# Optimization experiments

Measured on AMD Instinct MI355X. Metric: run time of the kernel, lower is better.

The kernel has to match this reference:

```python
import jax, jax.numpy as jnp
import numpy as np

B, N, S, K, NDIM, HID = 2, 8192, 1024, 32, 3, 256


def _sincos_embed(pos, dim):
    # pos: (..., ndim) continuous coordinates -> (..., dim) sincos embedding
    ndim = pos.shape[-1]
    emb_dim_per_dim = dim // ndim
    half = emb_dim_per_dim // 2
    freq = jnp.exp(jnp.arange(half, dtype=pos.dtype) * (-np.log(10000.0) / (half - 1)))
    embs = []
    for i in range(ndim):
        e = pos[..., i:i + 1] * freq  # (..., half)
        embs.append(jnp.concatenate([jnp.sin(e), jnp.cos(e)], axis=-1))
    x = jnp.concatenate(embs, axis=-1)  # (..., ndim*2*half)
    pad = dim - x.shape[-1]
    if pad > 0:
        x = jnp.pad(x, [(0, 0)] * (x.ndim - 1) + [(0, pad)])
    return x


def setup_inputs() -> dict:
    key = jax.random.key(0)
    ks = jax.random.split(key, 8)
    input_pos = jax.random.normal(ks[0], (B, N, NDIM), dtype=jnp.float32)
    supernode_idxs = jax.random.randint(ks[1], (S,), 0, N)
    # lecun_normal-style init (stddev = 1/sqrt(fan_in)), zero bias (torch/flax Dense default bias=0)
    w_in = jax.random.normal(ks[2], (NDIM, HID), dtype=jnp.float32) / np.sqrt(NDIM)
    b_in = jnp.zeros((HID,), jnp.float32)
    w1 = jax.random.normal(ks[3], (HID, HID), dtype=jnp.float32) / np.sqrt(HID)
    b1 = jnp.zeros((HID,), jnp.float32)
    w2 = jax.random.normal(ks[4], (HID, HID), dtype=jnp.float32) / np.sqrt(HID)
    b2 = jnp.zeros((HID,), jnp.float32)
    return {"input_pos": input_pos, "supernode_idxs": supernode_idxs,
            "w_in": w_in, "b_in": b_in, "w1": w1, "b1": b1, "w2": w2, "b2": b2}


def reference(input_pos, supernode_idxs, w_in, b_in, w1, b1, w2, b2):
    def knn(x):  # x: (N, ndim)
        # Euclidean distance from each supernode to every point: (S, N).
        # Same values as rows of the full NxN cdist the original materializes.
        d = jnp.sqrt(jnp.sum((x[supernode_idxs][:, None, :] - x[None, :, :]) ** 2, axis=-1))
        nbr = jnp.argsort(d, axis=1)[:, :K]  # (S, K)
        return x[nbr]  # (S, K, ndim)

    coords = jax.vmap(knn)(input_pos)  # (B, S, K, ndim)
    proj = coords @ w_in + b_in                         # (B, S, K, HID)
    pe = _sincos_embed(coords, HID)                     # (B, S, K, HID)
    h = proj + pe
    h = jax.nn.gelu(h @ w1 + b1) @ w2 + b2              # message MLP
    return jnp.mean(h, axis=-2)                         # (B, S, HID)
```

## Files before the change

kernel.cpp:

```cpp
#include <hip/hip_runtime.h>
#include <hip/hip_bf16.h>
#include <math.h>

#define BB   2
#define NN   8192
#define SS   1024
#define KK   32
#define HID  256
#define NTH  256
#define PPT  32
#define SENT 0xFFFFFFFFFFFFFFFFULL
#define LDB  264
#define WFE  65536

typedef unsigned long long u64;
typedef unsigned int       u32;
typedef short bf16x8 __attribute__((ext_vector_type(8)));
typedef float f32x4  __attribute__((ext_vector_type(4)));

#define CSW(SI) { const u64 mn = x < (SI) ? x : (SI); const u64 mx = x < (SI) ? (SI) : x; (SI) = mn; x = mx; }
#define INS(KV) { u64 x = (KV); CSW(s0) CSW(s1) CSW(s2) CSW(s3) }

__device__ __forceinline__ float tanh_fast(float y) {
    const float e = __expf(2.0f * y);
    const float r = __builtin_amdgcn_rcpf(e + 1.0f);
    return fmaf(-2.0f, r, 1.0f);
}

__device__ __forceinline__ short bf_bits(float f) {
    const __hip_bfloat16 h = __float2bfloat16(f);
    short s;
    __builtin_memcpy(&s, &h, 2);
    return s;
}

__device__ __forceinline__ int mbcnt64(u64 m) {
    return (int)__builtin_amdgcn_mbcnt_hi((u32)(m >> 32),
           __builtin_amdgcn_mbcnt_lo((u32)m, 0u));
}

__global__ void prep_w(const float* __restrict__ w1, const float* __restrict__ w2,
                       __hip_bfloat16* __restrict__ wf) {
    const int idx = blockIdx.x * 256 + threadIdx.x;
    const int j   = idx & 7;
    const int l   = (idx >> 3) & 63;
    const int ntg = (idx >> 9) & 15;
    const int ks  = (idx >> 13) & 7;
    const int mat = idx >> 16;
    const int k = ks * 32 + (l >> 4) * 8 + j;
    const int n = ntg * 16 + (l & 15);
    const float v = (mat ? w2 : w1)[k * HID + n];
    const __hip_bfloat16 hi = __float2bfloat16(v);
    const float res = v - __bfloat162float(hi);
    const size_t s0 = (size_t)mat * 131072 + ((size_t)((ks*16 + ntg)*2) * 64 + l) * 8 + j;
    wf[s0]       = hi;
    wf[s0 + 512] = __float2bfloat16(res);
}

__global__ __launch_bounds__(NTH, 8)
void snp_kernel(const float* __restrict__ pos,
                const int*   __restrict__ snidx,
                const float* __restrict__ w_in,
                const float* __restrict__ b_in,
                const float* __restrict__ b1,
                const float* __restrict__ b2,
                const __hip_bfloat16* __restrict__ wf,
                float*       __restrict__ out)
{
    const int bs   = blockIdx.x;
    const int b    = bs / SS;
    const int s    = bs - b * SS;
    const int t    = threadIdx.x;
    const int lane = t & 63;
    const int wv   = t >> 6;

    __shared__ __align__(16) short h0b[KK][LDB];
    __shared__ u64   wl[4 * KK];
    __shared__ int   nbr[KK];
    __shared__ __align__(16) float nbc[4 * KK];

    const float* posb = pos + (size_t)b * (NN * 3);
    const int   sp = snidx[s];
    const float sx = posb[sp*3 + 0];
    const float sy = posb[sp*3 + 1];
    const float sz = posb[sp*3 + 2];

    u64 s0=SENT,s1=SENT,s2=SENT,s3=SENT;
#pragma unroll 4
    for (int c = 0; c < PPT; ++c) {
        const int i = c * NTH + t;
        const float dx = __fsub_rn(sx, posb[i*3 + 0]);
        const float dy = __fsub_rn(sy, posb[i*3 + 1]);
        const float dz = __fsub_rn(sz, posb[i*3 + 2]);
        const float sq = __fadd_rn(__fadd_rn(__fmul_rn(dx,dx), __fmul_rn(dy,dy)),
                                   __fmul_rn(dz,dz));
        const u64 kv = ((u64)__float_as_uint(__fsqrt_rn(sq)) << 13) | (u32)i;
        INS(kv);
    }

    {
        u64 L = 0;
        for (int bit = 43; bit >= 13; --bit) {
            const u64 cand = L | (1ull << bit);
            const int cnt = __popcll(__ballot(s0 < cand)) + __popcll(__ballot(s1 < cand))
                          + __popcll(__ballot(s2 < cand)) + __popcll(__ballot(s3 < cand));
            if (cnt < 32) L = cand;
        }
        u64 TH = L + (1ull << 13);
        {
            const int cnt = __popcll(__ballot(s0 < TH)) + __popcll(__ballot(s1 < TH))
                          + __popcll(__ballot(s2 < TH)) + __popcll(__ballot(s3 < TH));
            if (cnt != 32) {
                for (int bit = 12; bit >= 0; --bit) {
                    const u64 cand = L | (1ull << bit);
                    const int c2 = __popcll(__ballot(s0 < cand)) + __popcll(__ballot(s1 < cand))
                                 + __popcll(__ballot(s2 < cand)) + __popcll(__ballot(s3 < cand));
                    if (c2 < 32) L = cand;
                }
                TH = L + 1;
            }
        }
        const bool b0 = s0 < TH, b1 = s1 < TH, b2 = s2 < TH, b3 = s3 < TH;
        const int csel = (int)b0 + (int)b1 + (int)b2 + (int)b3;

        if (__ballot(csel == 4) != 0ull) {
            int nv = 4;
#pragma unroll 1
            for (int it = 0; it < KK; ++it) {
                u64 m = s0;
#pragma unroll
                for (int off = 32; off > 0; off >>= 1) {
                    const u64 o = __shfl_xor(m, off, 64);
                    m = o < m ? o : m;
                }
                if (lane == 0) wl[wv*KK + it] = m;
                if (s0 == m) {
                    s0=s1; s1=s2; s2=s3; s3=SENT;
                    if (--nv == 0) {
                        const u64 last = m;
                        s0=s1=s2=s3=SENT;
#pragma unroll 4
                        for (int c = 0; c < PPT; ++c) {
                            const int i = c * NTH + t;
                            const float dx = __fsub_rn(sx, posb[i*3 + 0]);
                            const float dy = __fsub_rn(sy, posb[i*3 + 1]);
                            const float dz = __fsub_rn(sz, posb[i*3 + 2]);
                            const float sq = __fadd_rn(__fadd_rn(__fmul_rn(dx,dx), __fmul_rn(dy,dy)),
                                                       __fmul_rn(dz,dz));
                            u64 kv = ((u64)__float_as_uint(__fsqrt_rn(sq)) << 13) | (u32)i;
                            kv = kv > last ? kv : SENT;
                            INS(kv);
                        }
                        nv = (int)(s0!=SENT)+(int)(s1!=SENT)+(int)(s2!=SENT)+(int)(s3!=SENT);
                    }
                }
            }
        } else {
            const u64 m0 = __ballot(b0), m1 = __ballot(b1),
                      m2 = __ballot(b2), m3 = __ballot(b3);
            const int pos2 = mbcnt64(m0) + mbcnt64(m1) + mbcnt64(m2) + mbcnt64(m3);
            u64* wwl = &wl[wv * KK];
            if (b0) wwl[pos2]     = s0;
            if (b1) wwl[pos2 + 1] = s1;
            if (b2) wwl[pos2 + 2] = s2;
            if (b3) wwl[pos2 + 3] = s3;
        }
    }
    __syncthreads();

    if (t < 64) {
        const u64 k0 = wl[lane], k1 = wl[64 + lane];
        u64 L = 0;
        for (int bit = 43; bit >= 13; --bit) {
            const u64 cand = L | (1ull << bit);
            const int cnt = __popcll(__ballot(k0 < cand)) + __popcll(__ballot(k1 < cand));
            if (cnt < 32) L = cand;
        }
        u64 TH = L + (1ull << 13);
        {
            const int cnt = __popcll(__ballot(k0 < TH)) + __popcll(__ballot(k1 < TH));
            if (cnt != 32) {
                for (int bit = 12; bit >= 0; --bit) {
                    const u64 cand = L | (1ull << bit);
                    const int c2 = __popcll(__ballot(k0 < cand)) + __popcll(__ballot(k1 < cand));
                    if (c2 < 32) L = cand;
                }
                TH = L + 1;
            }
        }
        const bool c0 = k0 < TH, c1 = k1 < TH;
        const int p = mbcnt64(__ballot(c0)) + mbcnt64(__ballot(c1));
        if (c0) nbr[p]            = (int)(k0 & 8191u);
        if (c1) nbr[p + (int)c0]  = (int)(k1 & 8191u);
    }
    __syncthreads();

    if (t < KK * 3) {
        const int k = t / 3, d = t - 3 * k;
        nbc[k * 4 + d] = posb[(size_t)nbr[k] * 3 + d];
    }
    __syncthreads();

    {
        const int  c     = t;
        const int  dimi  = c / 84;
        const int  cc    = c - dimi * 84;
        const bool hasPe = c < 252;
        const bool isCos = cc >= 42;
        const int  f     = isCos ? cc - 42 : cc;
        const float fcoef = (float)(-9.210340371976184 / 41.0);
        const float freqv = expf((float)f * fcoef);
        const int  di    = hasPe ? dimi : 0;

        const float wi0 = w_in[0*HID + c];
        const float wi1 = w_in[1*HID + c];
        const float wi2 = w_in[2*HID + c];
        const float bi  = b_in[c];

#pragma unroll 4
        for (int k = 0; k < KK; ++k) {
            const float4 xv4 = *(const float4*)&nbc[k * 4];
            const float x0 = xv4.x, x1 = xv4.y, x2 = xv4.z;
            float v = fmaf(x2, wi2, fmaf(x1, wi1, fmaf(x0, wi0, bi)));
            if (hasPe) {
                const float xv  = (di == 0) ? x0 : ((di == 1) ? x1 : x2);
                const float ang = xv * freqv;
                v += isCos ? __cosf(ang) : __sinf(ang);
            }
            h0b[k][c] = bf_bits(v);
        }
    }
    __syncthreads();

    const int lr = lane & 15;
    const int lg = lane >> 4;
    const int nbase = wv * 64;

    const short* arow0 = &h0b[lr][lg * 8];
    const short* arow1 = &h0b[16 + lr][lg * 8];
    const __hip_bfloat16* wb1 = wf + (size_t)wv * 4096 + lane * 8;
    const __hip_bfloat16* wb2 = wb1 + 2 * WFE;

    f32x4 acc[2][4];

    {
#pragma unroll
        for (int nt = 0; nt < 4; ++nt) {
            const float bias = b1[nbase + nt*16 + lr];
            const f32x4 bv = {bias, bias, bias, bias};
            acc[0][nt] = bv; acc[1][nt] = bv;
        }
#pragma unroll 1
        for (int ks = 0; ks < 8; ++ks) {
            const bf16x8 af0 = *(const bf16x8*)(arow0 + ks * 32);
            const bf16x8 af1 = *(const bf16x8*)(arow1 + ks * 32);
            const __hip_bfloat16* p = wb1 + ks * 16384;
#pragma unroll
            for (int nt = 0; nt < 4; ++nt) {
                const bf16x8 bh = *(const bf16x8*)(p + nt * 1024);
                acc[0][nt] = __builtin_amdgcn_mfma_f32_16x16x32_bf16(af0, bh, acc[0][nt], 0,0,0);
                acc[1][nt] = __builtin_amdgcn_mfma_f32_16x16x32_bf16(af1, bh, acc[1][nt], 0,0,0);
                const bf16x8 bl = *(const bf16x8*)(p + nt * 1024 + 512);
                acc[0][nt] = __builtin_amdgcn_mfma_f32_16x16x32_bf16(af0, bl, acc[0][nt], 0,0,0);
                acc[1][nt] = __builtin_amdgcn_mfma_f32_16x16x32_bf16(af1, bl, acc[1][nt], 0,0,0);
            }
        }
    }
    __syncthreads();

    {
        const float kA = 0.7978845608028654f;
#pragma unroll
        for (int mt = 0; mt < 2; ++mt)
#pragma unroll
        for (int nt = 0; nt < 4; ++nt)
#pragma unroll
        for (int r = 0; r < 4; ++r) {
            const float x  = acc[mt][nt][r];
            const float x3 = x * x * x;
            const float tv = tanh_fast(kA * fmaf(0.044715f, x3, x));
            h0b[mt*16 + lg*4 + r][nbase + nt*16 + lr] = bf_bits(0.5f * x * (1.0f + tv));
        }
    }
    __syncthreads();

    {
        const f32x4 z = {0.f, 0.f, 0.f, 0.f};
#pragma unroll
        for (int nt = 0; nt < 4; ++nt) { acc[0][nt] = z; acc[1][nt] = z; }
#pragma unroll 1
        for (int ks = 0; ks < 8; ++ks) {
            const bf16x8 af0 = *(const bf16x8*)(arow0 + ks * 32);
            const bf16x8 af1 = *(const bf16x8*)(arow1 + ks * 32);
            const __hip_bfloat16* p = wb2 + ks * 16384;
#pragma unroll
            for (int nt = 0; nt < 4; ++nt) {
                const bf16x8 bh = *(const bf16x8*)(p + nt * 1024);
                acc[0][nt] = __builtin_amdgcn_mfma_f32_16x16x32_bf16(af0, bh, acc[0][nt], 0,0,0);
                acc[1][nt] = __builtin_amdgcn_mfma_f32_16x16x32_bf16(af1, bh, acc[1][nt], 0,0,0);
                const bf16x8 bl = *(const bf16x8*)(p + nt * 1024 + 512);
                acc[0][nt] = __builtin_amdgcn_mfma_f32_16x16x32_bf16(af0, bl, acc[0][nt], 0,0,0);
                acc[1][nt] = __builtin_amdgcn_mfma_f32_16x16x32_bf16(af1, bl, acc[1][nt], 0,0,0);
            }
        }
    }

#pragma unroll
    for (int nt = 0; nt < 4; ++nt) {
        float ssum = 0.0f;
#pragma unroll
        for (int mt = 0; mt < 2; ++mt)
#pragma unroll
            for (int r = 0; r < 4; ++r) ssum += acc[mt][nt][r];
        ssum += __shfl_xor(ssum, 16, 64);
        ssum += __shfl_xor(ssum, 32, 64);
        if (lane < 16) {
            const int ch = nbase + nt*16 + lane;
            out[(size_t)bs * HID + ch] = fmaf(ssum, 1.0f / KK, b2[ch]);
        }
    }
}

extern "C" void kernel_launch(void* const* d_in, const int* in_sizes, int n_in,
                              void* d_out, int out_size, void* d_ws, size_t ws_size,
                              hipStream_t stream) {
    const float* pos  = (const float*)d_in[0];
    const int*   sni  = (const int*)  d_in[1];
    const float* w_in = (const float*)d_in[2];
    const float* b_in = (const float*)d_in[3];
    const float* w1   = (const float*)d_in[4];
    const float* b1   = (const float*)d_in[5];
    const float* w2   = (const float*)d_in[6];
    const float* b2   = (const float*)d_in[7];
    float* out = (float*)d_out;
    __hip_bfloat16* wf = (__hip_bfloat16*)d_ws;
    (void)ws_size; (void)in_sizes; (void)n_in; (void)out_size;

    hipLaunchKernelGGL(prep_w, dim3(2 * WFE / 256), dim3(256), 0, stream, w1, w2, wf);
    hipLaunchKernelGGL(snp_kernel, dim3(BB * SS), dim3(NTH), 0, stream,
                       pos, sni, w_in, b_in, b1, b2, wf, out);
}
```

Baseline: 86.57 us.

## Double block size to 512 threads, splitting KNN scan and MLP columns across eight waves

Raises the block from 4 to 8 waves. Each thread now scans half as many points, the neighbour-selection wave merges eight per-wave candidate lists, and each wave computes half as many output-column tiles in both MFMA GEMMs. The aim is more latency hiding and parallel work per supernode, shortening the serial distance scan. In exchange, the final selection does more ballots, and keeping __launch_bounds__(NTH, 8) at 512 threads may squeeze registers or limit occupancy.

```diff
diff --git a/kernel.cpp b/kernel.cpp
--- a/kernel.cpp
+++ b/kernel.cpp
@@ -7,8 +7,9 @@
 #define SS   1024
 #define KK   32
 #define HID  256
-#define NTH  256
-#define PPT  32
+#define NTH  512
+#define NWV  8
+#define PPT  16
 #define SENT 0xFFFFFFFFFFFFFFFFULL
 #define LDB  264
 #define WFE  65536
@@ -75,7 +76,7 @@
     const int wv   = t >> 6;
 
     __shared__ __align__(16) short h0b[KK][LDB];
-    __shared__ u64   wl[4 * KK];
+    __shared__ u64   wl[NWV * KK];
     __shared__ int   nbr[KK];
     __shared__ __align__(16) float nbc[4 * KK];
 
@@ -169,29 +170,37 @@
     __syncthreads();
 
     if (t < 64) {
-        const u64 k0 = wl[lane], k1 = wl[64 + lane];
+        const u64 k0 = wl[lane],       k1 = wl[64 + lane];
+        const u64 k2 = wl[128 + lane], k3 = wl[192 + lane];
         u64 L = 0;
         for (int bit = 43; bit >= 13; --bit) {
             const u64 cand = L | (1ull << bit);
-            const int cnt = __popcll(__ballot(k0 < cand)) + __popcll(__ballot(k1 < cand));
+            const int cnt = __popcll(__ballot(k0 < cand)) + __popcll(__ballot(k1 < cand))
+                          + __popcll(__ballot(k2 < cand)) + __popcll(__ballot(k3 < cand));
             if (cnt < 32) L = cand;
         }
         u64 TH = L + (1ull << 13);
         {
-            const int cnt = __popcll(__ballot(k0 < TH)) + __popcll(__ballot(k1 < TH));
+            const int cnt = __popcll(__ballot(k0 < TH)) + __popcll(__ballot(k1 < TH))
+                          + __popcll(__ballot(k2 < TH)) + __popcll(__ballot(k3 < TH));
             if (cnt != 32) {
                 for (int bit = 12; bit >= 0; --bit) {
                     const u64 cand = L | (1ull << bit);
-                    const int c2 = __popcll(__ballot(k0 < cand)) + __popcll(__ballot(k1 < cand));
+                    const int c2 = __popcll(__ballot(k0 < cand)) + __popcll(__ballot(k1 < cand))
+                                 + __popcll(__ballot(k2 < cand)) + __popcll(__ballot(k3 < cand));
                     if (c2 < 32) L = cand;
                 }
                 TH = L + 1;
             }
         }
-        const bool c0 = k0 < TH, c1 = k1 < TH;
-        const int p = mbcnt64(__ballot(c0)) + mbcnt64(__ballot(c1));
-        if (c0) nbr[p]            = (int)(k0 & 8191u);
-        if (c1) nbr[p + (int)c0]  = (int)(k1 & 8191u);
+        const bool c0 = k0 < TH, c1 = k1 < TH, c2 = k2 < TH, c3 = k3 < TH;
+        const int p = mbcnt64(__ballot(c0)) + mbcnt64(__ballot(c1))
+                    + mbcnt64(__ballot(c2)) + mbcnt64(__ballot(c3));
+        int q = p;
+        if (c0) { nbr[q] = (int)(k0 & 8191u); ++q; }
+        if (c1) { nbr[q] = (int)(k1 & 8191u); ++q; }
+        if (c2) { nbr[q] = (int)(k2 & 8191u); ++q; }
+        if (c3) { nbr[q] = (int)(k3 & 8191u); }
     }
     __syncthreads();
 
@@ -202,7 +211,8 @@
     __syncthreads();
 
     {
-        const int  c     = t;
+        const int  c     = t & 255;
+        const int  kh    = (t >> 8) * 16;
         const int  dimi  = c / 84;
         const int  cc    = c - dimi * 84;
         const bool hasPe = c < 252;
@@ -218,7 +228,8 @@
         const float bi  = b_in[c];
 
 #pragma unroll 4
-        for (int k = 0; k < KK; ++k) {
+        for (int kk = 0; kk < 16; ++kk) {
+            const int k = kh + kk;
             const float4 xv4 = *(const float4*)&nbc[k * 4];
             const float x0 = xv4.x, x1 = xv4.y, x2 = xv4.z;
             float v = fmaf(x2, wi2, fmaf(x1, wi1, fmaf(x0, wi0, bi)));
@@ -234,18 +245,18 @@
 
     const int lr = lane & 15;
     const int lg = lane >> 4;
-    const int nbase = wv * 64;
+    const int nbase = wv * 32;
 
     const short* arow0 = &h0b[lr][lg * 8];
     const short* arow1 = &h0b[16 + lr][lg * 8];
-    const __hip_bfloat16* wb1 = wf + (size_t)wv * 4096 + lane * 8;
+    const __hip_bfloat16* wb1 = wf + (size_t)wv * 2048 + lane * 8;
     const __hip_bfloat16* wb2 = wb1 + 2 * WFE;
 
-    f32x4 acc[2][4];
-
-    {
-#pragma unroll
-        for (int nt = 0; nt < 4; ++nt) {
+    f32x4 acc[2][2];
+
+    {
+#pragma unroll
+        for (int nt = 0; nt < 2; ++nt) {
             const float bias = b1[nbase + nt*16 + lr];
             const f32x4 bv = {bias, bias, bias, bias};
             acc[0][nt] = bv; acc[1][nt] = bv;
@@ -256,7 +267,7 @@
             const bf16x8 af1 = *(const bf16x8*)(arow1 + ks * 32);
             const __hip_bfloat16* p = wb1 + ks * 16384;
 #pragma unroll
-            for (int nt = 0; nt < 4; ++nt) {
+            for (int nt = 0; nt < 2; ++nt) {
                 const bf16x8 bh = *(const bf16x8*)(p + nt * 1024);
                 acc[0][nt] = __builtin_amdgcn_mfma_f32_16x16x32_bf16(af0, bh, acc[0][nt], 0,0,0);
                 acc[1][nt] = __builtin_amdgcn_mfma_f32_16x16x32_bf16(af1, bh, acc[1][nt], 0,0,0);
@@ -273,7 +284,7 @@
 #pragma unroll
         for (int mt = 0; mt < 2; ++mt)
 #pragma unroll
-        for (int nt = 0; nt < 4; ++nt)
+        for (int nt = 0; nt < 2; ++nt)
 #pragma unroll
         for (int r = 0; r < 4; ++r) {
             const float x  = acc[mt][nt][r];
@@ -287,14 +298,14 @@
     {
         const f32x4 z = {0.f, 0.f, 0.f, 0.f};
 #pragma unroll
-        for (int nt = 0; nt < 4; ++nt) { acc[0][nt] = z; acc[1][nt] = z; }
+        for (int nt = 0; nt < 2; ++nt) { acc[0][nt] = z; acc[1][nt] = z; }
 #pragma unroll 1
         for (int ks = 0; ks < 8; ++ks) {
             const bf16x8 af0 = *(const bf16x8*)(arow0 + ks * 32);
             const bf16x8 af1 = *(const bf16x8*)(arow1 + ks * 32);
             const __hip_bfloat16* p = wb2 + ks * 16384;
 #pragma unroll
-            for (int nt = 0; nt < 4; ++nt) {
+            for (int nt = 0; nt < 2; ++nt) {
                 const bf16x8 bh = *(const bf16x8*)(p + nt * 1024);
                 acc[0][nt] = __builtin_amdgcn_mfma_f32_16x16x32_bf16(af0, bh, acc[0][nt], 0,0,0);
                 acc[1][nt] = __builtin_amdgcn_mfma_f32_16x16x32_bf16(af1, bh, acc[1][nt], 0,0,0);
@@ -306,7 +317,7 @@
     }
 
 #pragma unroll
-    for (int nt = 0; nt < 4; ++nt) {
+    for (int nt = 0; nt < 2; ++nt) {
         float ssum = 0.0f;
 #pragma unroll
         for (int mt = 0; mt < 2; ++mt)
```

New measurement: 104.0 us. 1.2x slower.

## Process two supernodes per block to reuse MLP weight fragments

Applied to the files above, without the earlier changes.

Each block now handles two supernodes, with half the threads (128) running the kNN scan for each, so every thread covers 64 points instead of 32. The MLP phase stacks 64 neighbor rows and issues four MFMA row tiles per weight fragment load, halving global weight traffic per token. The cost is a longer serial distance scan per thread, more accumulator registers, twice the shared memory, launch bounds lowered from 8 to 4 blocks per SM, and half as many blocks.

```diff
diff --git a/kernel.cpp b/kernel.cpp
--- a/kernel.cpp
+++ b/kernel.cpp
@@ -8,7 +8,7 @@
 #define KK   32
 #define HID  256
 #define NTH  256
-#define PPT  32
+#define PPT  64
 #define SENT 0xFFFFFFFFFFFFFFFFULL
 #define LDB  264
 #define WFE  65536
@@ -57,7 +57,7 @@
     wf[s0 + 512] = __float2bfloat16(res);
 }
 
-__global__ __launch_bounds__(NTH, 8)
+__global__ __launch_bounds__(NTH, 4)
 void snp_kernel(const float* __restrict__ pos,
                 const int*   __restrict__ snidx,
                 const float* __restrict__ w_in,
@@ -67,20 +67,23 @@
                 const __hip_bfloat16* __restrict__ wf,
                 float*       __restrict__ out)
 {
-    const int bs   = blockIdx.x;
-    const int b    = bs / SS;
-    const int s    = bs - b * SS;
+    const int tk0  = blockIdx.x * 2;
+    const int b    = tk0 / SS;
+    const int s0i  = tk0 - b * SS;
     const int t    = threadIdx.x;
     const int lane = t & 63;
     const int wv   = t >> 6;
-
-    __shared__ __align__(16) short h0b[KK][LDB];
+    const int tok  = t >> 7;
+    const int pl   = t & 127;
+
+    __shared__ __align__(16) short h0b[2 * KK][LDB];
     __shared__ u64   wl[4 * KK];
-    __shared__ int   nbr[KK];
-    __shared__ __align__(16) float nbc[4 * KK];
+    __shared__ int   nbr[2 * KK];
+    __shared__ __align__(16) float nbc[2 * 4 * KK];
 
     const float* posb = pos + (size_t)b * (NN * 3);
-    const int   sp = snidx[s];
+    const int  spA = snidx[s0i], spB = snidx[s0i + 1];
+    const int  sp  = tok ? spB : spA;
     const float sx = posb[sp*3 + 0];
     const float sy = posb[sp*3 + 1];
     const float sz = posb[sp*3 + 2];
@@ -88,7 +91,7 @@
     u64 s0=SENT,s1=SENT,s2=SENT,s3=SENT;
 #pragma unroll 4
     for (int c = 0; c < PPT; ++c) {
-        const int i = c * NTH + t;
+        const int i = c * 128 + pl;
         const float dx = __fsub_rn(sx, posb[i*3 + 0]);
         const float dy = __fsub_rn(sy, posb[i*3 + 1]);
         const float dz = __fsub_rn(sz, posb[i*3 + 2]);
@@ -141,7 +144,7 @@
                         s0=s1=s2=s3=SENT;
 #pragma unroll 4
                         for (int c = 0; c < PPT; ++c) {
-                            const int i = c * NTH + t;
+                            const int i = c * 128 + pl;
                             const float dx = __fsub_rn(sx, posb[i*3 + 0]);
                             const float dy = __fsub_rn(sy, posb[i*3 + 1]);
                             const float dz = __fsub_rn(sz, posb[i*3 + 2]);
@@ -168,34 +171,28 @@
     }
     __syncthreads();
 
-    if (t < 64) {
-        const u64 k0 = wl[lane], k1 = wl[64 + lane];
+    if (t < 128) {
+        const u64 k0 = wl[wv * 64 + lane];
         u64 L = 0;
         for (int bit = 43; bit >= 13; --bit) {
             const u64 cand = L | (1ull << bit);
-            const int cnt = __popcll(__ballot(k0 < cand)) + __popcll(__ballot(k1 < cand));
-            if (cnt < 32) L = cand;
+            if (__popcll(__ballot(k0 < cand)) < 32) L = cand;
         }
         u64 TH = L + (1ull << 13);
-        {
-            const int cnt = __popcll(__ballot(k0 < TH)) + __popcll(__ballot(k1 < TH));
-            if (cnt != 32) {
-                for (int bit = 12; bit >= 0; --bit) {
-                    const u64 cand = L | (1ull << bit);
-                    const int c2 = __popcll(__ballot(k0 < cand)) + __popcll(__ballot(k1 < cand));
-                    if (c2 < 32) L = cand;
-                }
-                TH = L + 1;
-            }
-        }
-        const bool c0 = k0 < TH, c1 = k1 < TH;
-        const int p = mbcnt64(__ballot(c0)) + mbcnt64(__ballot(c1));
-        if (c0) nbr[p]            = (int)(k0 & 8191u);
-        if (c1) nbr[p + (int)c0]  = (int)(k1 & 8191u);
-    }
-    __syncthreads();
-
-    if (t < KK * 3) {
+        if (__popcll(__ballot(k0 < TH)) != 32) {
+            for (int bit = 12; bit >= 0; --bit) {
+                const u64 cand = L | (1ull << bit);
+                if (__popcll(__ballot(k0 < cand)) < 32) L = cand;
+            }
+            TH = L + 1;
+        }
+        const bool c0 = k0 < TH;
+        const int p = mbcnt64(__ballot(c0));
+        if (c0) nbr[wv * KK + p] = (int)(k0 & 8191u);
+    }
+    __syncthreads();
+
+    if (t < 2 * KK * 3) {
         const int k = t / 3, d = t - 3 * k;
         nbc[k * 4 + d] = posb[(size_t)nbr[k] * 3 + d];
     }
@@ -218,7 +215,7 @@
         const float bi  = b_in[c];
 
 #pragma unroll 4
-        for (int k = 0; k < KK; ++k) {
+        for (int k = 0; k < 2 * KK; ++k) {
             const float4 xv4 = *(const float4*)&nbc[k * 4];
             const float x0 = xv4.x, x1 = xv4.y, x2 = xv4.z;
             float v = fmaf(x2, wi2, fmaf(x1, wi1, fmaf(x0, wi0, bi)));
@@ -238,31 +235,39 @@
 
     const short* arow0 = &h0b[lr][lg * 8];
     const short* arow1 = &h0b[16 + lr][lg * 8];
+    const short* arow2 = &h0b[32 + lr][lg * 8];
+    const short* arow3 = &h0b[48 + lr][lg * 8];
     const __hip_bfloat16* wb1 = wf + (size_t)wv * 4096 + lane * 8;
     const __hip_bfloat16* wb2 = wb1 + 2 * WFE;
 
-    f32x4 acc[2][4];
+    f32x4 acc[4][4];
 
     {
 #pragma unroll
         for (int nt = 0; nt < 4; ++nt) {
             const float bias = b1[nbase + nt*16 + lr];
             const f32x4 bv = {bias, bias, bias, bias};
-            acc[0][nt] = bv; acc[1][nt] = bv;
+            acc[0][nt] = bv; acc[1][nt] = bv; acc[2][nt] = bv; acc[3][nt] = bv;
         }
 #pragma unroll 1
         for (int ks = 0; ks < 8; ++ks) {
             const bf16x8 af0 = *(const bf16x8*)(arow0 + ks * 32);
             const bf16x8 af1 = *(const bf16x8*)(arow1 + ks * 32);
+            const bf16x8 af2 = *(const bf16x8*)(arow2 + ks * 32);
+            const bf16x8 af3 = *(const bf16x8*)(arow3 + ks * 32);
             const __hip_bfloat16* p = wb1 + ks * 16384;
 #pragma unroll
             for (int nt = 0; nt < 4; ++nt) {
                 const bf16x8 bh = *(const bf16x8*)(p + nt * 1024);
                 acc[0][nt] = __builtin_amdgcn_mfma_f32_16x16x32_bf16(af0, bh, acc[0][nt], 0,0,0);
                 acc[1][nt] = __builtin_amdgcn_mfma_f32_16x16x32_bf16(af1, bh, acc[1][nt], 0,0,0);
+                acc[2][nt] = __builtin_amdgcn_mfma_f32_16x16x32_bf16(af2, bh, acc[2][nt], 0,0,0);
+                acc[3][nt] = __builtin_amdgcn_mfma_f32_16x16x32_bf16(af3, bh, acc[3][nt], 0,0,0);
                 const bf16x8 bl = *(const bf16x8*)(p + nt * 1024 + 512);
                 acc[0][nt] = __builtin_amdgcn_mfma_f32_16x16x32_bf16(af0, bl, acc[0][nt], 0,0,0);
                 acc[1][nt] = __builtin_amdgcn_mfma_f32_16x16x32_bf16(af1, bl, acc[1][nt], 0,0,0);
+                acc[2][nt] = __builtin_amdgcn_mfma_f32_16x16x32_bf16(af2, bl, acc[2][nt], 0,0,0);
+                acc[3][nt] = __builtin_amdgcn_mfma_f32_16x16x32_bf16(af3, bl, acc[3][nt], 0,0,0);
             }
         }
     }
@@ -271,7 +276,7 @@
     {
         const float kA = 0.7978845608028654f;
 #pragma unroll
-        for (int mt = 0; mt < 2; ++mt)
+        for (int mt = 0; mt < 4; ++mt)
 #pragma unroll
         for (int nt = 0; nt < 4; ++nt)
 #pragma unroll
@@ -287,36 +292,47 @@
     {
         const f32x4 z = {0.f, 0.f, 0.f, 0.f};
 #pragma unroll
-        for (int nt = 0; nt < 4; ++nt) { acc[0][nt] = z; acc[1][nt] = z; }
+        for (int nt = 0; nt < 4; ++nt) {
+            acc[0][nt] = z; acc[1][nt] = z; acc[2][nt] = z; acc[3][nt] = z;
+        }
 #pragma unroll 1
         for (int ks = 0; ks < 8; ++ks) {
             const bf16x8 af0 = *(const bf16x8*)(arow0 + ks * 32);
             const bf16x8 af1 = *(const bf16x8*)(arow1 + ks * 32);
+            const bf16x8 af2 = *(const bf16x8*)(arow2 + ks * 32);
+            const bf16x8 af3 = *(const bf16x8*)(arow3 + ks * 32);
             const __hip_bfloat16* p = wb2 + ks * 16384;
 #pragma unroll
             for (int nt = 0; nt < 4; ++nt) {
                 const bf16x8 bh = *(const bf16x8*)(p + nt * 1024);
                 acc[0][nt] = __builtin_amdgcn_mfma_f32_16x16x32_bf16(af0, bh, acc[0][nt], 0,0,0);
                 acc[1][nt] = __builtin_amdgcn_mfma_f32_16x16x32_bf16(af1, bh, acc[1][nt], 0,0,0);
+                acc[2][nt] = __builtin_amdgcn_mfma_f32_16x16x32_bf16(af2, bh, acc[2][nt], 0,0,0);
+                acc[3][nt] = __builtin_amdgcn_mfma_f32_16x16x32_bf16(af3, bh, acc[3][nt], 0,0,0);
                 const bf16x8 bl = *(const bf16x8*)(p + nt * 1024 + 512);
                 acc[0][nt] = __builtin_amdgcn_mfma_f32_16x16x32_bf16(af0, bl, acc[0][nt], 0,0,0);
                 acc[1][nt] = __builtin_amdgcn_mfma_f32_16x16x32_bf16(af1, bl, acc[1][nt], 0,0,0);
+                acc[2][nt] = __builtin_amdgcn_mfma_f32_16x16x32_bf16(af2, bl, acc[2][nt], 0,0,0);
+                acc[3][nt] = __builtin_amdgcn_mfma_f32_16x16x32_bf16(af3, bl, acc[3][nt], 0,0,0);
             }
         }
     }
 
 #pragma unroll
     for (int nt = 0; nt < 4; ++nt) {
-        float ssum = 0.0f;
-#pragma unroll
-        for (int mt = 0; mt < 2; ++mt)
-#pragma unroll
-            for (int r = 0; r < 4; ++r) ssum += acc[mt][nt][r];
-        ssum += __shfl_xor(ssum, 16, 64);
-        ssum += __shfl_xor(ssum, 32, 64);
+        float sumA = 0.0f, sumB = 0.0f;
+#pragma unroll
+        for (int r = 0; r < 4; ++r) {
+            sumA += acc[0][nt][r] + acc[1][nt][r];
+            sumB += acc[2][nt][r] + acc[3][nt][r];
+        }
+        sumA += __shfl_xor(sumA, 16, 64); sumA += __shfl_xor(sumA, 32, 64);
+        sumB += __shfl_xor(sumB, 16, 64); sumB += __shfl_xor(sumB, 32, 64);
         if (lane < 16) {
             const int ch = nbase + nt*16 + lane;
-            out[(size_t)bs * HID + ch] = fmaf(ssum, 1.0f / KK, b2[ch]);
+            const float bb = b2[ch];
+            out[(size_t)tk0 * HID + ch]       = fmaf(sumA, 1.0f / KK, bb);
+            out[(size_t)(tk0 + 1) * HID + ch] = fmaf(sumB, 1.0f / KK, bb);
         }
     }
 }
@@ -337,6 +353,6 @@
     (void)ws_size; (void)in_sizes; (void)n_in; (void)out_size;
 
     hipLaunchKernelGGL(prep_w, dim3(2 * WFE / 256), dim3(256), 0, stream, w1, w2, wf);
-    hipLaunchKernelGGL(snp_kernel, dim3(BB * SS), dim3(NTH), 0, stream,
+    hipLaunchKernelGGL(snp_kernel, dim3(BB * SS / 2), dim3(NTH), 0, stream,
                        pos, sni, w_in, b_in, b1, b2, wf, out);
 }
```

New measurement: 86.40 us. Within noise of the previous version (-0.2%).
